# Kernel optimization log

Hardware: AMD Instinct MI355X
Metric: run time of the kernel (lower is better)

Reference implementation:

```python
import jax, jax.numpy as jnp
import numpy as np

T, D, H, E, TOP_K = 4096, 512, 2048, 16, 2


def setup_inputs() -> dict:
    key = jax.random.key(0)
    ks = jax.random.split(key, 4)
    x = jax.random.normal(ks[0], (T, D), dtype=jnp.float32)
    Wg = jax.random.normal(ks[1], (D, E), dtype=jnp.float32) * 0.02
    bg = jnp.zeros((E,), dtype=jnp.float32)
    W1 = jax.random.normal(ks[2], (E, D, H), dtype=jnp.float32) * 0.02
    b1 = jnp.zeros((E, H), dtype=jnp.float32)
    W2 = jax.random.normal(ks[3], (E, H, D), dtype=jnp.float32) * 0.02
    b2 = jnp.zeros((E, D), dtype=jnp.float32)
    return {"x": x, "Wg": Wg, "bg": bg, "W1": W1, "b1": b1, "W2": W2, "b2": b2}


def reference(x, Wg, bg, W1, b1, W2, b2):
    # NaiveGate: linear -> top-k -> softmax over the k selected logits
    logits = x @ Wg + bg                               # [T, E]
    gate_vals, gate_idx = jax.lax.top_k(logits, TOP_K)  # [T, k]
    gate_score = jax.nn.softmax(gate_vals, axis=-1)     # returned by gate; NOT applied to output (faithful to source)

    # combine weights: how many top-k slots of each token map to each expert
    counts = jax.nn.one_hot(gate_idx, E, dtype=x.dtype).sum(axis=1)  # [T, E]

    # Expert FFN (grouped GEMM expressed densely over the fixed expert axis)
    h = jax.nn.gelu(jnp.einsum('td,edh->eth', x, W1) + b1[:, None, :])  # [E, T, H]
    y = jnp.einsum('eth,ehd->etd', h, W2) + b2[:, None, :]              # [E, T, D]

    # Combine: unweighted sum over the token's top-k experts (matches .sum(dim=1) in source)
    out = jnp.einsum('etd,te->td', y, counts)                            # [T, D]
    return out, gate_idx, gate_score
```

## Files before the change

### kernel.cpp

```cpp
#include <hip/hip_runtime.h>
#include <math.h>

#define T_ 4096
#define D_ 512
#define H_ 2048
#define E_ 16
#define RCAP 10240

typedef short bf16x8 __attribute__((ext_vector_type(8)));
typedef float f32x4 __attribute__((ext_vector_type(4)));

__device__ __forceinline__ unsigned short f2bf(float f) {
  union { float f; unsigned u; } v; v.f = f;
  unsigned r = v.u + 0x7fffu + ((v.u >> 16) & 1u);
  return (unsigned short)(r >> 16);
}
__device__ __forceinline__ float bf2f(unsigned short u) {
  union { unsigned u; float f; } v; v.u = ((unsigned)u) << 16;
  return v.f;
}
__device__ __forceinline__ void gload_lds16(const unsigned short* g, unsigned short* l) {
  __builtin_amdgcn_global_load_lds((const __attribute__((address_space(1))) void*)g,
                                   (__attribute__((address_space(3))) void*)l, 16, 0, 0);
}

__global__ __launch_bounds__(256) void gate_kernel(const float* __restrict__ x,
                                                   const float* __restrict__ Wg,
                                                   const float* __restrict__ bg,
                                                   float* __restrict__ out,
                                                   int* __restrict__ tok2e) {
  __shared__ float wgl[D_ * E_];
  for (int i = threadIdx.x; i < D_ * E_ / 4; i += 256)
    *(float4*)&wgl[i * 4] = ((const float4*)Wg)[i];
  __syncthreads();
  const int lane = threadIdx.x & 63;
  const int t = blockIdx.x * 4 + (threadIdx.x >> 6);
  const int e = lane & 15, q = lane >> 4;
  const float4* x4 = (const float4*)(x + (size_t)t * D_ + q * 128);
  float acc = 0.f;
#pragma unroll 4
  for (int i = 0; i < 32; ++i) {
    float4 v = x4[i];
    const float* wp = &wgl[(q * 128 + i * 4) * E_ + e];
    acc += v.x * wp[0];
    acc += v.y * wp[E_];
    acc += v.z * wp[2 * E_];
    acc += v.w * wp[3 * E_];
  }
  acc += __shfl_xor(acc, 16);
  acc += __shfl_xor(acc, 32);
  const float logit = acc + bg[e];
  float v1 = logit; int i1 = e;
#pragma unroll
  for (int s = 1; s < 16; s <<= 1) {
    float ov = __shfl_xor(v1, s); int oi = __shfl_xor(i1, s);
    if (ov > v1 || (ov == v1 && oi < i1)) { v1 = ov; i1 = oi; }
  }
  float v2 = (e == i1) ? -INFINITY : logit; int i2 = e;
#pragma unroll
  for (int s = 1; s < 16; s <<= 1) {
    float ov = __shfl_xor(v2, s); int oi = __shfl_xor(i2, s);
    if (ov > v2 || (ov == v2 && oi < i2)) { v2 = ov; i2 = oi; }
  }
  if (lane == 0) {
    const float ed = __expf(v2 - v1);
    const float inv = 1.f / (1.f + ed);
    const size_t gidx = (size_t)T_ * D_;
    out[gidx + t * 2]     = (float)i1;
    out[gidx + t * 2 + 1] = (float)i2;
    out[gidx + T_ * 2 + t * 2]     = inv;
    out[gidx + T_ * 2 + t * 2 + 1] = ed * inv;
    tok2e[t * 2] = i1; tok2e[t * 2 + 1] = i2;
  }
}

__global__ void count_kernel(const int* __restrict__ tok2e,
                             int* __restrict__ cnt2,
                             int* __restrict__ offs, int* __restrict__ tileoff,
                             int* __restrict__ rowbuf) {
  __shared__ int h[E_];
  if (threadIdx.x < E_) h[threadIdx.x] = 0;
  __syncthreads();
  for (int i = threadIdx.x; i < 2 * T_; i += 256) atomicAdd(&h[tok2e[i]], 1);
  __syncthreads();
  if (threadIdx.x == 0) {
    int o = 0, to = 0;
    offs[0] = 0; tileoff[0] = 0;
    for (int e = 0; e < E_; ++e) {
      int mt = (h[e] + 127) >> 7;
      o += mt << 7; to += mt;
      offs[e + 1] = o; tileoff[e + 1] = to;
    }
  }
  for (int i = threadIdx.x; i < E_ * 16; i += 256) cnt2[i] = 0;
  for (int i = threadIdx.x; i < RCAP; i += 256) rowbuf[i] = -1;
}

__global__ void scatter_kernel(const int* __restrict__ tok2e, int* __restrict__ cnt2,
                               const int* __restrict__ offs, int* __restrict__ rowbuf,
                               int* __restrict__ tok2row) {
  const int t = blockIdx.x * blockDim.x + threadIdx.x;
#pragma unroll
  for (int k = 0; k < 2; ++k) {
    int e = tok2e[t * 2 + k];
    int slot = atomicAdd(&cnt2[e * 16], 1);
    int row = offs[e] + slot;
    rowbuf[row] = t;
    tok2row[t * 2 + k] = row;
  }
}

__global__ void gather_kernel(const float* __restrict__ x,
                              const int* __restrict__ rowbuf,
                              const int* __restrict__ offs,
                              unsigned short* __restrict__ xg) {
  const int row = blockIdx.x;
  if (row >= offs[16]) return;
  const int t = rowbuf[row];
  const int lane = threadIdx.x;
  float4 a = make_float4(0.f, 0.f, 0.f, 0.f), b = a;
  if (t >= 0) {
    const float4* p = (const float4*)(x + (size_t)t * D_ + lane * 8);
    a = p[0]; b = p[1];
  }
  unsigned w0 = f2bf(a.x) | (f2bf(a.y) << 16);
  unsigned w1 = f2bf(a.z) | (f2bf(a.w) << 16);
  unsigned w2 = f2bf(b.x) | (f2bf(b.y) << 16);
  unsigned w3 = f2bf(b.z) | (f2bf(b.w) << 16);
  *(uint4*)(xg + (size_t)row * D_ + lane * 8) = make_uint4(w0, w1, w2, w3);
}

template <int K, int N>
__global__ __launch_bounds__(256) void wtrans_kernel(const float* __restrict__ src,
                                                     unsigned short* __restrict__ dst) {
  __shared__ unsigned short tile[64][72];
  const int e = blockIdx.z;
  const int n0 = blockIdx.x << 6, k0 = blockIdx.y << 6;
  const int tid = threadIdx.x;
  const int tr = tid >> 4, tc = (tid & 15) << 2;
  const float* s = src + ((size_t)e * K + k0) * N + n0;
#pragma unroll
  for (int p = 0; p < 4; ++p) {
    float4 v = *(const float4*)(s + (size_t)(tr + p * 16) * N + tc);
    tile[tc + 0][tr + p * 16] = f2bf(v.x);
    tile[tc + 1][tr + p * 16] = f2bf(v.y);
    tile[tc + 2][tr + p * 16] = f2bf(v.z);
    tile[tc + 3][tr + p * 16] = f2bf(v.w);
  }
  __syncthreads();
  const int wr = tid >> 2, wc = (tid & 3) << 4;
  unsigned short* d = dst + ((size_t)e * N + n0 + wr) * K + k0 + wc;
  *(uint4*)d       = *(const uint4*)&tile[wr][wc];
  *(uint4*)(d + 8) = *(const uint4*)&tile[wr][wc + 8];
}

template <int KDIM, int NTOT, int NTILE, bool GELU>
__global__ __launch_bounds__(256) void ffn_gemm(
    const unsigned short* __restrict__ A_g, const unsigned short* __restrict__ Bt_g,
    const float* __restrict__ bias_g, unsigned short* __restrict__ out_g,
    const int* __restrict__ offs, const int* __restrict__ tileoff) {
  constexpr int JN = NTILE / 32;
  constexpr int BRPW = NTILE / 4;
  __shared__ unsigned short As[128 * 64];
  __shared__ unsigned short Bs[NTILE * 64];
  const int mt = blockIdx.x;
  if (mt >= tileoff[16]) return;
  int e = 0;
  while (tileoff[e + 1] <= mt) ++e;
  const int row0 = offs[e] + ((mt - tileoff[e]) << 7);
  const int n0 = blockIdx.y * NTILE;
  const int tid = threadIdx.x;
  const int lane = tid & 63;
  const int w = tid >> 6;
  const int m_off = (w & 1) << 6;
  const int n_off = (tid >> 7) * (NTILE / 2);

  f32x4 acc[4][JN];
#pragma unroll
  for (int i = 0; i < 4; ++i)
#pragma unroll
    for (int j = 0; j < JN; ++j) acc[i][j] = (f32x4){0.f, 0.f, 0.f, 0.f};

  const int r_in = lane >> 3;
  const int cbg = (lane & 7) ^ r_in;
  const unsigned short* gA = A_g + (size_t)(row0 + w * 32 + r_in) * KDIM + cbg * 8;
  const unsigned short* gB = Bt_g + ((size_t)e * NTOT + n0 + w * BRPW + r_in) * KDIM + cbg * 8;
  unsigned short* lA = &As[w * 32 * 64];
  unsigned short* lB = &Bs[w * BRPW * 64];

  const int q = lane >> 4, fr = lane & 15;

  for (int k0 = 0; k0 < KDIM; k0 += 64) {
#pragma unroll
    for (int j = 0; j < 4; ++j)
      gload_lds16(gA + (size_t)j * 8 * KDIM + k0, lA + j * 8 * 64);
#pragma unroll
    for (int j = 0; j < BRPW / 8; ++j)
      gload_lds16(gB + (size_t)j * 8 * KDIM + k0, lB + j * 8 * 64);
    __syncthreads();
#pragma unroll
    for (int kk = 0; kk < 64; kk += 32) {
      bf16x8 af[4], bfr[JN];
#pragma unroll
      for (int i = 0; i < 4; ++i) {
        const int r = m_off + i * 16 + fr;
        const int sw = ((((kk >> 3) + q) ^ (r & 7)) << 3);
        af[i] = *(const bf16x8*)&As[r * 64 + sw];
      }
#pragma unroll
      for (int j = 0; j < JN; ++j) {
        const int r = n_off + j * 16 + fr;
        const int sw = ((((kk >> 3) + q) ^ (r & 7)) << 3);
        bfr[j] = *(const bf16x8*)&Bs[r * 64 + sw];
      }
#pragma unroll
      for (int i = 0; i < 4; ++i)
#pragma unroll
        for (int j = 0; j < JN; ++j)
          acc[i][j] = __builtin_amdgcn_mfma_f32_16x16x32_bf16(af[i], bfr[j], acc[i][j], 0, 0, 0);
    }
    __syncthreads();
  }
  const float* bias = bias_g + (size_t)e * NTOT;
#pragma unroll
  for (int j = 0; j < JN; ++j) {
    const int col = n0 + n_off + j * 16 + fr;
    const float bv = bias[col];
#pragma unroll
    for (int i = 0; i < 4; ++i) {
      const int rbase = row0 + m_off + i * 16 + (q << 2);
      f32x4 v = acc[i][j];
#pragma unroll
      for (int r = 0; r < 4; ++r) {
        float y = v[r] + bv;
        if (GELU) y = 0.5f * y * (1.f + erff(y * 0.70710678118f));
        out_g[(size_t)(rbase + r) * NTOT + col] = f2bf(y);
      }
    }
  }
}

__global__ void combine_kernel(const unsigned short* __restrict__ ybuf,
                               const int* __restrict__ tok2row,
                               float* __restrict__ out) {
  const int t = blockIdx.x, lane = threadIdx.x;
  const int rA = tok2row[t * 2], rB = tok2row[t * 2 + 1];
  const uint4 va = *(const uint4*)(ybuf + (size_t)rA * D_ + lane * 8);
  const uint4 vb = *(const uint4*)(ybuf + (size_t)rB * D_ + lane * 8);
  const unsigned short* pa = (const unsigned short*)&va;
  const unsigned short* pb = (const unsigned short*)&vb;
  float o[8];
#pragma unroll
  for (int i = 0; i < 8; ++i) o[i] = bf2f(pa[i]) + bf2f(pb[i]);
  float4* po = (float4*)(out + (size_t)t * D_ + lane * 8);
  po[0] = make_float4(o[0], o[1], o[2], o[3]);
  po[1] = make_float4(o[4], o[5], o[6], o[7]);
}

extern "C" void kernel_launch(void* const* d_in, const int* in_sizes, int n_in,
                              void* d_out, int out_size, void* d_ws, size_t ws_size,
                              hipStream_t stream) {
  const float* x  = (const float*)d_in[0];
  const float* Wg = (const float*)d_in[1];
  const float* bg = (const float*)d_in[2];
  const float* W1 = (const float*)d_in[3];
  const float* b1 = (const float*)d_in[4];
  const float* W2 = (const float*)d_in[5];
  const float* b2 = (const float*)d_in[6];
  float* out = (float*)d_out;
  char* ws = (char*)d_ws;

  int* cnt2    = (int*)(ws);
  int* offs    = (int*)(ws + 2048);
  int* tileoff = (int*)(ws + 3072);
  int* tok2e   = (int*)(ws + 4096);
  int* tok2row = (int*)(ws + 4096 + 32768);
  int* rowbuf  = (int*)(ws + 4096 + 65536);
  unsigned short* xg   = (unsigned short*)(ws + (1 << 20));
  unsigned short* ybuf = xg;
  unsigned short* hbuf = (unsigned short*)(ws + (size_t)(12 << 20));
  unsigned short* Wt   = (unsigned short*)(ws + (size_t)(52 << 20));

  gate_kernel<<<T_ / 4, 256, 0, stream>>>(x, Wg, bg, out, tok2e);
  count_kernel<<<1, 256, 0, stream>>>(tok2e, cnt2, offs, tileoff, rowbuf);
  scatter_kernel<<<T_ / 256, 256, 0, stream>>>(tok2e, cnt2, offs, rowbuf, tok2row);
  gather_kernel<<<RCAP, 64, 0, stream>>>(x, rowbuf, offs, xg);
  wtrans_kernel<D_, H_><<<dim3(H_ / 64, D_ / 64, E_), 256, 0, stream>>>(W1, Wt);
  ffn_gemm<512, 2048, 128, true><<<dim3(80, 16), 256, 0, stream>>>(xg, Wt, b1, hbuf, offs, tileoff);
  wtrans_kernel<H_, D_><<<dim3(D_ / 64, H_ / 64, E_), 256, 0, stream>>>(W2, Wt);
  ffn_gemm<2048, 512, 64, false><<<dim3(80, 8), 256, 0, stream>>>(hbuf, Wt, b2, ybuf, offs, tileoff);
  combine_kernel<<<T_, 64, 0, stream>>>(ybuf, tok2row, out);
}
```

Baseline: 294.2 us.

## Fuse scatter/gather, use fast GELU, and stage GEMM epilogue through LDS

After: 280.8 us. 1.05x faster.

```diff
diff --git a/kernel.cpp b/kernel.cpp
--- a/kernel.cpp
+++ b/kernel.cpp
@@ -22,6 +22,10 @@
 __device__ __forceinline__ void gload_lds16(const unsigned short* g, unsigned short* l) {
   __builtin_amdgcn_global_load_lds((const __attribute__((address_space(1))) void*)g,
                                    (__attribute__((address_space(3))) void*)l, 16, 0, 0);
+}
+__device__ __forceinline__ float gelu_fast(float y) {
+  float s2 = 1.5957691216f * (y + 0.044715f * y * y * y);
+  return y * __builtin_amdgcn_rcpf(1.f + __expf(-s2));
 }
 
 __global__ __launch_bounds__(256) void gate_kernel(const float* __restrict__ x,
@@ -76,8 +80,7 @@
 
 __global__ void count_kernel(const int* __restrict__ tok2e,
                              int* __restrict__ cnt2,
-                             int* __restrict__ offs, int* __restrict__ tileoff,
-                             int* __restrict__ rowbuf) {
+                             int* __restrict__ offs, int* __restrict__ tileoff) {
   __shared__ int h[E_];
   if (threadIdx.x < E_) h[threadIdx.x] = 0;
   __syncthreads();
@@ -93,41 +96,31 @@
     }
   }
   for (int i = threadIdx.x; i < E_ * 16; i += 256) cnt2[i] = 0;
-  for (int i = threadIdx.x; i < RCAP; i += 256) rowbuf[i] = -1;
-}
-
-__global__ void scatter_kernel(const int* __restrict__ tok2e, int* __restrict__ cnt2,
-                               const int* __restrict__ offs, int* __restrict__ rowbuf,
-                               int* __restrict__ tok2row) {
-  const int t = blockIdx.x * blockDim.x + threadIdx.x;
-#pragma unroll
-  for (int k = 0; k < 2; ++k) {
-    int e = tok2e[t * 2 + k];
-    int slot = atomicAdd(&cnt2[e * 16], 1);
-    int row = offs[e] + slot;
-    rowbuf[row] = t;
-    tok2row[t * 2 + k] = row;
-  }
-}
-
-__global__ void gather_kernel(const float* __restrict__ x,
-                              const int* __restrict__ rowbuf,
-                              const int* __restrict__ offs,
-                              unsigned short* __restrict__ xg) {
-  const int row = blockIdx.x;
-  if (row >= offs[16]) return;
-  const int t = rowbuf[row];
-  const int lane = threadIdx.x;
-  float4 a = make_float4(0.f, 0.f, 0.f, 0.f), b = a;
-  if (t >= 0) {
-    const float4* p = (const float4*)(x + (size_t)t * D_ + lane * 8);
-    a = p[0]; b = p[1];
-  }
-  unsigned w0 = f2bf(a.x) | (f2bf(a.y) << 16);
-  unsigned w1 = f2bf(a.z) | (f2bf(a.w) << 16);
-  unsigned w2 = f2bf(b.x) | (f2bf(b.y) << 16);
-  unsigned w3 = f2bf(b.z) | (f2bf(b.w) << 16);
-  *(uint4*)(xg + (size_t)row * D_ + lane * 8) = make_uint4(w0, w1, w2, w3);
+}
+
+__global__ __launch_bounds__(256) void scatgath_kernel(
+    const float* __restrict__ x, const int* __restrict__ tok2e,
+    int* __restrict__ cnt2, const int* __restrict__ offs,
+    int* __restrict__ tok2row, unsigned short* __restrict__ xg) {
+  const int lane = threadIdx.x & 63;
+  const int t = blockIdx.x * 4 + (threadIdx.x >> 6);
+  int rA = 0, rB = 0;
+  if (lane == 0) {
+    const int e1 = tok2e[t * 2], e2 = tok2e[t * 2 + 1];
+    rA = offs[e1] + atomicAdd(&cnt2[e1 * 16], 1);
+    rB = offs[e2] + atomicAdd(&cnt2[e2 * 16], 1);
+    tok2row[t * 2] = rA; tok2row[t * 2 + 1] = rB;
+  }
+  rA = __shfl(rA, 0); rB = __shfl(rB, 0);
+  const float4* p = (const float4*)(x + (size_t)t * D_ + lane * 8);
+  const float4 a = p[0], b = p[1];
+  const unsigned w0 = f2bf(a.x) | (f2bf(a.y) << 16);
+  const unsigned w1 = f2bf(a.z) | (f2bf(a.w) << 16);
+  const unsigned w2 = f2bf(b.x) | (f2bf(b.y) << 16);
+  const unsigned w3 = f2bf(b.z) | (f2bf(b.w) << 16);
+  const uint4 val = make_uint4(w0, w1, w2, w3);
+  *(uint4*)(xg + (size_t)rA * D_ + lane * 8) = val;
+  *(uint4*)(xg + (size_t)rB * D_ + lane * 8) = val;
 }
 
 template <int K, int N>
@@ -221,22 +214,38 @@
     }
     __syncthreads();
   }
+
+  constexpr int W = NTILE / 2;
+  constexpr int LB = W / 8;
+  unsigned short* cbase;
+  if (NTILE == 128) cbase = (w < 2) ? &As[w * 4096] : &Bs[(w - 2) * 4096];
+  else              cbase = &As[w * 2048];
   const float* bias = bias_g + (size_t)e * NTOT;
 #pragma unroll
   for (int j = 0; j < JN; ++j) {
-    const int col = n0 + n_off + j * 16 + fr;
-    const float bv = bias[col];
+    const float bv = bias[n0 + n_off + j * 16 + fr];
 #pragma unroll
     for (int i = 0; i < 4; ++i) {
-      const int rbase = row0 + m_off + i * 16 + (q << 2);
       f32x4 v = acc[i][j];
 #pragma unroll
       for (int r = 0; r < 4; ++r) {
         float y = v[r] + bv;
-        if (GELU) y = 0.5f * y * (1.f + erff(y * 0.70710678118f));
-        out_g[(size_t)(rbase + r) * NTOT + col] = f2bf(y);
+        if (GELU) y = gelu_fast(y);
+        const int lr = i * 16 + (q << 2) + r;
+        const int lc = j * 16 + fr;
+        const int phys = (lc >> 3) ^ (lr & (LB - 1));
+        cbase[lr * W + phys * 8 + (lc & 7)] = f2bf(y);
       }
     }
+  }
+  __syncthreads();
+#pragma unroll
+  for (int it = 0; it < LB; ++it) {
+    const int lr = it * (64 / LB) + (lane / LB);
+    const int bl = lane % LB;
+    const int phys = bl ^ (lr & (LB - 1));
+    const uint4 val = *(const uint4*)&cbase[lr * W + phys * 8];
+    *(uint4*)&out_g[(size_t)(row0 + m_off + lr) * NTOT + n0 + n_off + bl * 8] = val;
   }
 }
 
@@ -275,16 +284,14 @@
   int* tileoff = (int*)(ws + 3072);
   int* tok2e   = (int*)(ws + 4096);
   int* tok2row = (int*)(ws + 4096 + 32768);
-  int* rowbuf  = (int*)(ws + 4096 + 65536);
   unsigned short* xg   = (unsigned short*)(ws + (1 << 20));
   unsigned short* ybuf = xg;
   unsigned short* hbuf = (unsigned short*)(ws + (size_t)(12 << 20));
   unsigned short* Wt   = (unsigned short*)(ws + (size_t)(52 << 20));
 
   gate_kernel<<<T_ / 4, 256, 0, stream>>>(x, Wg, bg, out, tok2e);
-  count_kernel<<<1, 256, 0, stream>>>(tok2e, cnt2, offs, tileoff, rowbuf);
-  scatter_kernel<<<T_ / 256, 256, 0, stream>>>(tok2e, cnt2, offs, rowbuf, tok2row);
-  gather_kernel<<<RCAP, 64, 0, stream>>>(x, rowbuf, offs, xg);
+  count_kernel<<<1, 256, 0, stream>>>(tok2e, cnt2, offs, tileoff);
+  scatgath_kernel<<<T_ / 4, 256, 0, stream>>>(x, tok2e, cnt2, offs, tok2row, xg);
   wtrans_kernel<D_, H_><<<dim3(H_ / 64, D_ / 64, E_), 256, 0, stream>>>(W1, Wt);
   ffn_gemm<512, 2048, 128, true><<<dim3(80, 16), 256, 0, stream>>>(xg, Wt, b1, hbuf, offs, tileoff);
   wtrans_kernel<H_, D_><<<dim3(D_ / 64, H_ / 64, E_), 256, 0, stream>>>(W2, Wt);
```
